# Kernel tuning notes

Hardware: AMD Instinct MI355X
Metric: run time of the kernel (lower is better)

Reference implementation:

```python
import jax, jax.numpy as jnp
import numpy as np

N = 50000        # nodes
E = 800000       # edges
R = 8            # relations
G = 64           # g_dim
H1 = 64          # h1_dim
H2 = 32          # h2_dim (per-head for transformer, output for sage)
HEADS = 4
EPS = 1e-5       # BatchNorm eps


def setup_inputs() -> dict:
    key = jax.random.key(0)
    ks = jax.random.split(key, 16)
    def rn(k, shape, scale=0.05):
        return jax.random.normal(k, shape, dtype=jnp.float32) * scale
    return {
        "node_features": jax.random.normal(ks[0], (N, G), dtype=jnp.float32),
        "node_type": jax.random.randint(ks[1], (N,), 0, 3),
        "edge_index": jax.random.randint(ks[2], (2, E), 0, N),
        "edge_type": jax.random.randint(ks[3], (E,), 0, R),
        # RGCNConv params (per-relation weight + root weight + bias)
        "rgcn_w": rn(ks[4], (R, G, H1)),
        "rgcn_root": rn(ks[5], (G, H1)),
        "rgcn_bias": jnp.zeros((H1,), jnp.float32),
        "bn1_g": jnp.ones((H1,), jnp.float32),
        "bn1_b": jnp.zeros((H1,), jnp.float32),
        # TransformerConv params (q/k/v projections + skip)
        "wq": rn(ks[6], (H1, HEADS * H2)), "bq": jnp.zeros((HEADS * H2,), jnp.float32),
        "wk": rn(ks[7], (H1, HEADS * H2)), "bk": jnp.zeros((HEADS * H2,), jnp.float32),
        "wv": rn(ks[8], (H1, HEADS * H2)), "bv": jnp.zeros((HEADS * H2,), jnp.float32),
        "wskip": rn(ks[9], (H1, HEADS * H2)), "bskip": jnp.zeros((HEADS * H2,), jnp.float32),
        "bn2_g": jnp.ones((HEADS * H2,), jnp.float32),
        "bn2_b": jnp.zeros((HEADS * H2,), jnp.float32),
        # SAGEConv params (lin_l on aggregated neighbors has bias; lin_r on root has none)
        "sage_wl": rn(ks[10], (HEADS * H2, H2)), "sage_bl": jnp.zeros((H2,), jnp.float32),
        "sage_wr": rn(ks[11], (HEADS * H2, H2)),
        "bn3_g": jnp.ones((H2,), jnp.float32),
        "bn3_b": jnp.zeros((H2,), jnp.float32),
    }


def _bn(x, g, b):
    # BatchNorm1d in training mode: biased batch statistics over nodes
    m = x.mean(0)
    v = x.var(0)
    return g * (x - m) * jax.lax.rsqrt(v + EPS) + b


def _match(res, d):
    # F.pad(res, (0, d - c)): pads with zeros if d > c, truncates if d < c
    c = res.shape[1]
    if d > c:
        return jnp.pad(res, ((0, 0), (0, d - c)))
    return res[:, :d]


def _forward(node_features, rgcn_w, rgcn_root, rgcn_bias, bn1_g, bn1_b,
             wq, bq, wk, bk, wv, bv, wskip, bskip, bn2_g, bn2_b,
             sage_wl, sage_bl, sage_wr, bn3_g, bn3_b,
             edge_index, edge_type):
    src, dst = edge_index[0], edge_index[1]
    x = node_features
    residual = x

    # ---- RGCNConv: per-relation transform, per-relation mean aggregation, sum over relations ----
    xr = jnp.einsum('nf,rfh->nrh', x, rgcn_w)            # [N,R,H1]
    msg = xr[src, edge_type]                              # [E,H1]
    seg = dst * R + edge_type                             # segment per (node, relation)
    sums = jax.ops.segment_sum(msg, seg, num_segments=N * R)
    cnt = jax.ops.segment_sum(jnp.ones((E,), msg.dtype), seg, num_segments=N * R)
    agg = (sums / jnp.maximum(cnt, 1.0)[:, None]).reshape(N, R, H1).sum(1)
    h = agg + x @ rgcn_root + rgcn_bias
    h = jax.nn.leaky_relu(_bn(h, bn1_g, bn1_b))
    x = h + _match(residual, h.shape[1])
    residual = x

    # ---- TransformerConv: edge softmax attention, concat heads, + skip projection ----
    q = (x @ wq + bq).reshape(N, HEADS, H2)
    k = (x @ wk + bk).reshape(N, HEADS, H2)
    v = (x @ wv + bv).reshape(N, HEADS, H2)
    logits = (q[dst] * k[src]).sum(-1) / jnp.sqrt(jnp.float32(H2))  # [E,HEADS]
    mx = jax.ops.segment_max(logits, dst, num_segments=N)
    ex = jnp.exp(logits - mx[dst])
    den = jax.ops.segment_sum(ex, dst, num_segments=N)
    alpha = ex / jnp.maximum(den[dst], 1e-16)
    out = jax.ops.segment_sum(alpha[:, :, None] * v[src], dst, num_segments=N)
    h = out.reshape(N, HEADS * H2) + x @ wskip + bskip
    h = jax.nn.leaky_relu(_bn(h, bn2_g, bn2_b))
    x = h + _match(residual, h.shape[1])
    residual = x

    # ---- SAGEConv: mean neighbor aggregation + root transform ----
    nsum = jax.ops.segment_sum(x[src], dst, num_segments=N)
    ncnt = jax.ops.segment_sum(jnp.ones((E,), x.dtype), dst, num_segments=N)
    nmean = nsum / jnp.maximum(ncnt, 1.0)[:, None]
    h = nmean @ sage_wl + sage_bl + x @ sage_wr
    h = jax.nn.leaky_relu(_bn(h, bn3_g, bn3_b))
    return h + _match(residual, h.shape[1])


def reference(node_features, node_type, edge_index, edge_type,
              rgcn_w, rgcn_root, rgcn_bias, bn1_g, bn1_b,
              wq, bq, wk, bk, wv, bv, wskip, bskip, bn2_g, bn2_b,
              sage_wl, sage_bl, sage_wr, bn3_g, bn3_b):
    # node_type is unused by the original forward
    return _forward(node_features, rgcn_w, rgcn_root, rgcn_bias, bn1_g, bn1_b,
                    wq, bq, wk, bk, wv, bv, wskip, bskip, bn2_g, bn2_b,
                    sage_wl, sage_bl, sage_wr, bn3_g, bn3_b,
                    edge_index, edge_type)
```

## Files before the change

kernel.cpp:

```cpp
#include <hip/hip_runtime.h>
#include <stdint.h>

#define NN 50000
#define NE 800000
#define NE4 (NE/4)
#define NR (NN*8)
#define SCAN_BS 512
#define NB2 782
#define INV_N (1.0f/50000.0f)
#define BN_EPS 1e-5f

typedef unsigned short ushort_t;
typedef unsigned char uchar_t;
typedef short bf16x8 __attribute__((ext_vector_type(8)));
typedef float f32x4 __attribute__((ext_vector_type(4)));
typedef float f32x2 __attribute__((ext_vector_type(2)));

__device__ __forceinline__ ushort_t f2bf(float f){
    unsigned int u = __float_as_uint(f);
    u += 0x7FFFu + ((u >> 16) & 1u);
    return (ushort_t)(u >> 16);
}
__device__ __forceinline__ float bf2f(ushort_t h){ return __uint_as_float(((unsigned int)h) << 16); }
__device__ __forceinline__ float bflo(unsigned int u){ return __uint_as_float(u << 16); }
__device__ __forceinline__ float bfhi(unsigned int u){ return __uint_as_float(u & 0xFFFF0000u); }

__device__ __forceinline__ unsigned int f4_to_fp8(float a, float b, float c, float d){
    int v = __builtin_amdgcn_cvt_pk_fp8_f32(a, b, 0, false);
    v = __builtin_amdgcn_cvt_pk_fp8_f32(c, d, v, true);
    return (unsigned int)v;
}
__device__ __forceinline__ void fp8_to_f4(unsigned int u, float& a, float& b, float& c, float& d){
    f32x2 lo = __builtin_amdgcn_cvt_pk_f32_fp8(u, false);
    f32x2 hi = __builtin_amdgcn_cvt_pk_f32_fp8(u, true);
    a = lo.x; b = lo.y; c = hi.x; d = hi.y;
}

__global__ void k_prep(const float* __restrict__ nf,
                       const float* __restrict__ rgcn_w, const float* __restrict__ root,
                       const float* __restrict__ wq, const float* __restrict__ wk,
                       const float* __restrict__ wv, const float* __restrict__ wsk,
                       const float* __restrict__ bq, const float* __restrict__ bk,
                       const float* __restrict__ bv, const float* __restrict__ bsk,
                       const float* __restrict__ wl, const float* __restrict__ wr,
                       const int* __restrict__ ei, const int* __restrict__ et,
                       int* __restrict__ deg, uint2* __restrict__ sr,
                       ushort_t* __restrict__ xb, uchar_t* __restrict__ xb8,
                       ushort_t* __restrict__ Wcat,
                       ushort_t* __restrict__ Wt2, float* __restrict__ bcat,
                       ushort_t* __restrict__ Wsage){
    int i = blockIdx.x*256 + threadIdx.x;
    if (i < NE4){
        int4 d = ((const int4*)(ei + NE))[i];
        int4 r = ((const int4*)et)[i];
        int s0 = d.x*8 + r.x, s1 = d.y*8 + r.y;
        int s2 = d.z*8 + r.z, s3 = d.w*8 + r.w;
        int r0 = atomicAdd(&deg[s0], 1);
        int r1 = atomicAdd(&deg[s1], 1);
        int r2 = atomicAdd(&deg[s2], 1);
        int r3 = atomicAdd(&deg[s3], 1);
        uint2* o = sr + (size_t)i*4;
        uint2 o0; o0.x = (unsigned)s0; o0.y = (unsigned)r0; o[0] = o0;
        uint2 o1; o1.x = (unsigned)s1; o1.y = (unsigned)r1; o[1] = o1;
        uint2 o2; o2.x = (unsigned)s2; o2.y = (unsigned)r2; o[2] = o2;
        uint2 o3; o3.x = (unsigned)s3; o3.y = (unsigned)r3; o[3] = o3;
        return;
    }
    int ii = i - NE4;
    const int NXB = NN*16;
    if (ii < NXB){
        float4 v = ((const float4*)nf)[ii];
        ushort4 h;
        h.x = f2bf(v.x); h.y = f2bf(v.y); h.z = f2bf(v.z); h.w = f2bf(v.w);
        ((ushort4*)xb)[ii] = h;
        ((unsigned int*)xb8)[ii] = f4_to_fp8(v.x, v.y, v.z, v.w);
        return;
    }
    int j = ii - NXB;
    if (j < 64*576){
        int h = j / 576, k = j - h*576;
        float v = (k < 512) ? rgcn_w[(size_t)k*64 + h] : root[(size_t)(k-512)*64 + h];
        Wcat[j] = f2bf(v);
    } else if (j < 64*576 + 512*64){
        int jj = j - 64*576;
        int c = jj >> 6, k = jj & 63;
        int mt = c >> 7, cc = c & 127;
        const float* W = (mt==0)?wq:(mt==1)?wk:(mt==2)?wv:wsk;
        Wt2[jj] = f2bf(W[(size_t)k*128 + cc]);
    } else if (j < 64*576 + 512*64 + 512){
        int c = j - (64*576 + 512*64);
        int mt = c >> 7, cc = c & 127;
        const float* B = (mt==0)?bq:(mt==1)?bk:(mt==2)?bv:bsk;
        bcat[c] = B[cc];
    } else if (j < 64*576 + 512*64 + 512 + 32*256){
        int jj = j - (64*576 + 512*64 + 512);
        int c = jj >> 8, k = jj & 255;
        float v = (k < 128) ? wr[(size_t)k*32 + c] : wl[(size_t)(k-128)*32 + c];
        Wsage[jj] = f2bf(v);
    }
}

__global__ void k_scan1(const int* __restrict__ deg, int* __restrict__ tmp, int* __restrict__ bsum){
    __shared__ int s[SCAN_BS];
    int t = threadIdx.x;
    int i = blockIdx.x*SCAN_BS + t;
    s[t] = (i < NR) ? deg[i] : 0;
    __syncthreads();
    for (int off = 1; off < SCAN_BS; off <<= 1){
        int add = (t >= off) ? s[t-off] : 0;
        __syncthreads();
        s[t] += add;
        __syncthreads();
    }
    if (i < NR) tmp[i] = s[t];
    if (t == SCAN_BS-1) bsum[blockIdx.x] = s[t];
}

__global__ void k_scan2(int* __restrict__ bsum){
    __shared__ int s[1024];
    int t = threadIdx.x;
    s[t] = (t < NB2) ? bsum[t] : 0;
    __syncthreads();
    for (int off = 1; off < 1024; off <<= 1){
        int v = (t >= off) ? s[t-off] : 0;
        __syncthreads();
        s[t] += v;
        __syncthreads();
    }
    if (t < NB2) bsum[t] = s[t];
}

__global__ void k_scan3(const int* __restrict__ tmp, const int* __restrict__ bsum, int* __restrict__ rs){
    int i = blockIdx.x*256 + threadIdx.x;
    if (i < NR){
        int b = i >> 9;
        int off = (b > 0) ? bsum[b-1] : 0;
        rs[i+1] = tmp[i] + off;
        if (i == 0) rs[0] = 0;
    }
}

__global__ void k_fill(const int* __restrict__ ei, const uint2* __restrict__ sr,
                       const int* __restrict__ rs, int* __restrict__ csr){
    int e = blockIdx.x*256 + threadIdx.x;
    if (e < NE){
        uint2 s = sr[e];
        csr[rs[s.x] + (int)s.y] = ei[e];
    }
}

__global__ __launch_bounds__(256) void rgcn_fused(const ushort_t* __restrict__ xb,
                                                  const uchar_t* __restrict__ xb8,
                                                  const int* __restrict__ rs,
                                                  const int* __restrict__ csr,
                                                  const ushort_t* __restrict__ Wcat,
                                                  const float* __restrict__ bias,
                                                  float* __restrict__ h1pre,
                                                  float* __restrict__ part1){
    __shared__ ushort_t Ml[16*520];
    int w = threadIdx.x >> 6, lane = threadIdx.x & 63;
    int quad = lane >> 4, l4 = lane & 15;
    int row0 = blockIdx.x * 16;
    int n0 = row0 + w*4;
    int rsel = (lane < 9 ? lane : 8);
    int rb = rs[n0*8 + rsel];
    int eb0 = __shfl(rb, 0);
    int dg0 = __shfl(rb, 8) - eb0;
    int idx = (lane < dg0) ? csr[eb0 + lane] : 0;
    for (int j = 0; j < 4; ++j){
        int lrow = (w*4 + j)*520;
        int ebase = __shfl(rb, 0);
        int enext = __shfl(rb, 8);
        int rb_next = 0, idxn = 0;
        if (j < 3){
            rb_next = rs[(n0 + j + 1)*8 + rsel];
            idxn = csr[min(enext + lane, NE - 1)];
        }
        int e0a = __shfl(rb, 2*quad);
        int e1a = __shfl(rb, 2*quad + 1);
        int e2a = __shfl(rb, 2*quad + 2);
        int oa = e0a - ebase;
        int la = e1a - e0a, lb = e2a - e1a;
        int tot = la + lb;
        int fastN = min(tot, max(64 - oa, 0));
        int ml = fastN;
        ml = max(ml, __shfl_xor(ml, 16));
        ml = max(ml, __shfl_xor(ml, 32));
        f32x2 aA0 = {0.f,0.f}, aA1 = {0.f,0.f};
        f32x2 aB0 = {0.f,0.f}, aB1 = {0.f,0.f};
        for (int i = 0; i < ml; i += 4){
            unsigned int uX[4];
#pragma unroll
            for (int u = 0; u < 4; ++u){
                int jj = i + u;
                int t = __shfl(idx, (oa + jj) & 63);
                t = (jj < fastN) ? t : 0;
                uX[u] = *(const unsigned int*)(xb8 + (size_t)t*64 + l4*4);
            }
#pragma unroll
            for (int u = 0; u < 4; ++u){
                int jj = i + u;
                unsigned int a = (jj < fastN) ? uX[u] : 0u;
                f32x2 lo = __builtin_amdgcn_cvt_pk_f32_fp8(a, false);
                f32x2 hi = __builtin_amdgcn_cvt_pk_f32_fp8(a, true);
                if (jj < la){ aA0 += lo; aA1 += hi; }
                else        { aB0 += lo; aB1 += hi; }
            }
        }
        for (int jj = min(la, fastN); jj < la; ++jj){
            int t = csr[e0a + jj];
            unsigned int a = *(const unsigned int*)(xb8 + (size_t)t*64 + l4*4);
            aA0 += __builtin_amdgcn_cvt_pk_f32_fp8(a, false);
            aA1 += __builtin_amdgcn_cvt_pk_f32_fp8(a, true);
        }
        for (int jj = max(la, fastN); jj < tot; ++jj){
            int t = csr[e0a + jj];
            unsigned int b = *(const unsigned int*)(xb8 + (size_t)t*64 + l4*4);
            aB0 += __builtin_amdgcn_cvt_pk_f32_fp8(b, false);
            aB1 += __builtin_amdgcn_cvt_pk_f32_fp8(b, true);
        }
        float inva = 1.f / fmaxf((float)la, 1.f);
        float invb = 1.f / fmaxf((float)lb, 1.f);
        ushort4 oA, oB;
        oA.x = f2bf(aA0.x*inva); oA.y = f2bf(aA0.y*inva); oA.z = f2bf(aA1.x*inva); oA.w = f2bf(aA1.y*inva);
        oB.x = f2bf(aB0.x*invb); oB.y = f2bf(aB0.y*invb); oB.z = f2bf(aB1.x*invb); oB.w = f2bf(aB1.y*invb);
        *(ushort4*)&Ml[lrow + (2*quad)*64 + l4*4] = oA;
        *(ushort4*)&Ml[lrow + (2*quad + 1)*64 + l4*4] = oB;
        if (j < 3){
            rb = rb_next;
            int ebn = __shfl(rb, 0);
            int dgn = __shfl(rb, 8) - ebn;
            idx = (lane < dgn) ? idxn : 0;
        }
    }
    __syncthreads();
    int m = l4;
    f32x4 acc = {};
#pragma unroll
    for (int kt = 0; kt < 18; ++kt){
        int kk = kt*32 + quad*8;
        bf16x8 a;
        if (kt < 16) a = *(const bf16x8*)&Ml[m*520 + kk];
        else         a = *(const bf16x8*)(xb + (size_t)(row0 + m)*64 + (kk - 512));
        bf16x8 b = *(const bf16x8*)(Wcat + (size_t)(w*16 + m)*576 + kk);
        acc = __builtin_amdgcn_mfma_f32_16x16x32_bf16(a, b, acc, 0, 0, 0);
    }
    int col = w*16 + m;
    float bz = bias[col];
    float s = 0.f, q = 0.f;
#pragma unroll
    for (int i = 0; i < 4; ++i){
        int rr = row0 + quad*4 + i;
        float y = acc[i] + bz;
        h1pre[(size_t)rr*64 + col] = y;
        s += y; q += y*y;
    }
    s += __shfl_xor(s, 16); q += __shfl_xor(q, 16);
    s += __shfl_xor(s, 32); q += __shfl_xor(q, 32);
    if (quad == 0){
        float* pg = part1 + (blockIdx.x & 31)*128;
        atomicAdd(&pg[col], s);
        atomicAdd(&pg[64 + col], q);
    }
}

#define QS 132
#define BS 68
__global__ __launch_bounds__(256) void gemm_qkvs(const float* __restrict__ h1pre,
                                                 const float* __restrict__ nf,
                                                 const float* __restrict__ part1,
                                                 const float* __restrict__ g1, const float* __restrict__ b1,
                                                 const ushort_t* __restrict__ Wt2,
                                                 const float* __restrict__ bcat,
                                                 ushort_t* __restrict__ qb,
                                                 uchar_t* __restrict__ kb8,
                                                 uchar_t* __restrict__ vb8,
                                                 ushort_t* __restrict__ sb){
    __shared__ ushort_t Bs[256*BS];
    __shared__ ushort_t pl[4][16*QS];
    __shared__ float sred[128];
    int w = threadIdx.x >> 6, lane = threadIdx.x & 63;
    int m = lane & 15, quad = lane >> 4;
    int r0 = blockIdx.x*64 + w*16;
    int row = r0 + m;
    {
        int t = threadIdx.x;
        if (t < 128){
            float acc = 0.f;
#pragma unroll
            for (int g = 0; g < 32; ++g) acc += part1[g*128 + t];
            sred[t] = acc;
        }
    }
    __syncthreads();
    bf16x8 afrag[2];
#pragma unroll
    for (int kt = 0; kt < 2; ++kt){
        int db = kt*32 + quad*8;
        bf16x8 f = (bf16x8){0,0,0,0,0,0,0,0};
        if (row < NN){
            float4 h0 = *(const float4*)(h1pre + (size_t)row*64 + db);
            float4 h1 = *(const float4*)(h1pre + (size_t)row*64 + db + 4);
            float4 n0 = *(const float4*)(nf + (size_t)row*64 + db);
            float4 n1 = *(const float4*)(nf + (size_t)row*64 + db + 4);
            float4 ga = *(const float4*)(g1 + db);
            float4 gb_ = *(const float4*)(g1 + db + 4);
            float4 ba = *(const float4*)(b1 + db);
            float4 bb_ = *(const float4*)(b1 + db + 4);
            float hh[8] = {h0.x,h0.y,h0.z,h0.w,h1.x,h1.y,h1.z,h1.w};
            float nn[8] = {n0.x,n0.y,n0.z,n0.w,n1.x,n1.y,n1.z,n1.w};
            float GG[8] = {ga.x,ga.y,ga.z,ga.w,gb_.x,gb_.y,gb_.z,gb_.w};
            float BB[8] = {ba.x,ba.y,ba.z,ba.w,bb_.x,bb_.y,bb_.z,bb_.w};
#pragma unroll
            for (int e = 0; e < 8; ++e){
                float mm = sred[db + e] * INV_N;
                float vv = sred[64 + db + e] * INV_N - mm*mm;
                float A = rsqrtf(fmaxf(vv, 0.f) + BN_EPS) * GG[e];
                float C = BB[e] - mm * A;
                float y = fmaf(hh[e], A, C);
                y = (y >= 0.f) ? y : 0.01f*y;
                f[e] = (short)f2bf(y + nn[e]);
            }
        }
        afrag[kt] = f;
    }
    for (int cg = 0; cg < 2; ++cg){
        __syncthreads();
        {
            int t = threadIdx.x;
            const ushort_t* wsrc = Wt2 + (size_t)cg*256*64;
#pragma unroll
            for (int u0 = 0; u0 < 8; ++u0){
                int u = u0*256 + t;
                int r = u >> 3, c8 = (u & 7)*8;
                *(uint4*)&Bs[r*BS + c8] = *(const uint4*)(wsrc + u*8);
            }
        }
        __syncthreads();
        f32x4 acc[16] = {};
#pragma unroll
        for (int kt = 0; kt < 2; ++kt){
            int kk = kt*32 + quad*8;
#pragma unroll
            for (int ct = 0; ct < 16; ++ct){
                bf16x8 b = *(const bf16x8*)&Bs[(size_t)(ct*16 + m)*BS + kk];
                acc[ct] = __builtin_amdgcn_mfma_f32_16x16x32_bf16(afrag[kt], b, acc[ct], 0, 0, 0);
            }
        }
#pragma unroll
        for (int ct = 0; ct < 8; ++ct){
            int g = cg*256 + ct*16 + m;
            float bz = bcat[g];
            int cc = g & 127;
#pragma unroll
            for (int i = 0; i < 4; ++i)
                pl[w][(quad*4 + i)*QS + cc] = f2bf(acc[ct][i] + bz);
        }
        if (cg == 0){
#pragma unroll
            for (int t = 0; t < 4; ++t){
                int u = t*64 + lane;
                int r = u >> 4, c = (u & 15)*8;
                int gr = r0 + r;
                if (gr < NN) *(uint4*)(qb + (size_t)gr*128 + c) = *(const uint4*)&pl[w][r*QS + c];
            }
        } else {
#pragma unroll
            for (int t = 0; t < 4; ++t){
                int u = t*64 + lane;
                int r = u >> 4, c = (u & 15)*8;
                int gr = r0 + r;
                if (gr < NN){
                    uint4 vv4 = *(const uint4*)&pl[w][r*QS + c];
                    uint2 o;
                    o.x = f4_to_fp8(bflo(vv4.x), bfhi(vv4.x), bflo(vv4.y), bfhi(vv4.y));
                    o.y = f4_to_fp8(bflo(vv4.z), bfhi(vv4.z), bflo(vv4.w), bfhi(vv4.w));
                    *(uint2*)(vb8 + (size_t)gr*128 + c) = o;
                }
            }
        }
#pragma unroll
        for (int ct = 8; ct < 16; ++ct){
            int g = cg*256 + ct*16 + m;
            float bz = bcat[g];
            int cc = g & 127;
#pragma unroll
            for (int i = 0; i < 4; ++i)
                pl[w][(quad*4 + i)*QS + cc] = f2bf(acc[ct][i] + bz);
        }
        if (cg == 0){
#pragma unroll
            for (int t = 0; t < 4; ++t){
                int u = t*64 + lane;
                int r = u >> 4, c = (u & 15)*8;
                int gr = r0 + r;
                if (gr < NN){
                    uint4 kk4 = *(const uint4*)&pl[w][r*QS + c];
                    uint2 o;
                    o.x = f4_to_fp8(bflo(kk4.x), bfhi(kk4.x), bflo(kk4.y), bfhi(kk4.y));
                    o.y = f4_to_fp8(bflo(kk4.z), bfhi(kk4.z), bflo(kk4.w), bfhi(kk4.w));
                    *(uint2*)(kb8 + (size_t)gr*128 + c) = o;
                }
            }
        } else {
#pragma unroll
            for (int t = 0; t < 4; ++t){
                int u = t*64 + lane;
                int r = u >> 4, c = (u & 15)*8;
                int gr = r0 + r;
                if (gr < NN) *(uint4*)(sb + (size_t)gr*128 + c) = *(const uint4*)&pl[w][r*QS + c];
            }
        }
    }
}

__global__ void k_red2(const float* __restrict__ part1, const float* __restrict__ part2,
                       float* __restrict__ bns){
    int t = threadIdx.x;
    float acc = 0.f;
    for (int g = 0; g < 64; ++g) acc += part2[g*256 + t];
    bns[128 + t] = acc;
    if (t < 128){
        float a1 = 0.f;
        for (int g = 0; g < 32; ++g) a1 += part1[g*128 + t];
        bns[t] = a1;
    }
}

__global__ __launch_bounds__(256) void sage_gemm(const ushort_t* __restrict__ x2b,
                                                 const ushort_t* __restrict__ nmeanb,
                                                 const ushort_t* __restrict__ Wsage,
                                                 const float* __restrict__ bl,
                                                 float* __restrict__ h3,
                                                 float* __restrict__ part3){
    int wv = threadIdx.x >> 6, lane = threadIdx.x & 63;
    int r0 = blockIdx.x*64 + wv*16;
    int m = lane & 15, quad = lane >> 4;
    int row = r0 + m;
    f32x4 acc[2] = {};
#pragma unroll
    for (int kt = 0; kt < 8; ++kt){
        int kk = kt*32 + quad*8;
        bf16x8 a;
        if (row < NN){
            const ushort_t* ap = (kt < 4) ? (x2b + (size_t)row*128 + kk)
                                          : (nmeanb + (size_t)row*128 + (kk - 128));
            a = *(const bf16x8*)ap;
        } else {
            a = (bf16x8){0,0,0,0,0,0,0,0};
        }
#pragma unroll
        for (int ct = 0; ct < 2; ++ct){
            bf16x8 b = *(const bf16x8*)(Wsage + (size_t)(ct*16 + m)*256 + kk);
            acc[ct] = __builtin_amdgcn_mfma_f32_16x16x32_bf16(a, b, acc[ct], 0, 0, 0);
        }
    }
    float s[2] = {0.f, 0.f}, q[2] = {0.f, 0.f};
#pragma unroll
    for (int ct = 0; ct < 2; ++ct){
        int col = ct*16 + m;
        float bz = bl[col];
#pragma unroll
        for (int i = 0; i < 4; ++i){
            int rr = r0 + quad*4 + i;
            if (rr < NN){
                float y = acc[ct][i] + bz;
                h3[(size_t)rr*32 + col] = y;
                s[ct] += y; q[ct] += y*y;
            }
        }
    }
#pragma unroll
    for (int ct = 0; ct < 2; ++ct){
        s[ct] += __shfl_xor(s[ct], 16); q[ct] += __shfl_xor(q[ct], 16);
        s[ct] += __shfl_xor(s[ct], 32); q[ct] += __shfl_xor(q[ct], 32);
    }
    if (quad == 0){
        float* pg = part3 + (blockIdx.x & 3)*64;
#pragma unroll
        for (int ct = 0; ct < 2; ++ct){
            int col = ct*16 + m;
            atomicAdd(&pg[col], s[ct]);
            atomicAdd(&pg[32 + col], q[ct]);
        }
    }
}

__device__ __forceinline__ float bn_leaky(float z, float m, float rsv, float g, float b){
    float y = (z - m) * rsv * g + b;
    return y >= 0.f ? y : 0.01f * y;
}

__global__ void bn_apply2(const float* __restrict__ h2, const float* __restrict__ h1pre,
                          const float* __restrict__ nf,
                          const float* __restrict__ g1, const float* __restrict__ b1,
                          const float* __restrict__ s1, const float* __restrict__ q1,
                          const float* __restrict__ g2, const float* __restrict__ b2,
                          const float* __restrict__ s2, const float* __restrict__ q2,
                          float* __restrict__ x2r, ushort_t* __restrict__ x2b,
                          uchar_t* __restrict__ x28){
    int i = blockIdx.x*256 + threadIdx.x;
    if (i >= NN*128) return;
    int n = i >> 7, c = i & 127;
    float m2 = s2[c] * INV_N;
    float v2 = q2[c] * INV_N - m2*m2;
    float rsv2 = rsqrtf(fmaxf(v2, 0.f) + BN_EPS);
    float val = bn_leaky(h2[i], m2, rsv2, g2[c], b2[c]);
    if (c < 64){
        float m1 = s1[c] * INV_N;
        float v1 = q1[c] * INV_N - m1*m1;
        float rsv1 = rsqrtf(fmaxf(v1, 0.f) + BN_EPS);
        val += bn_leaky(h1pre[(size_t)n*64 + c], m1, rsv1, g1[c], b1[c]) + nf[(size_t)n*64 + c];
    }
    if (c < 32) x2r[(size_t)n*32 + c] = val;
    x2b[i] = f2bf(val);
    int p = __builtin_amdgcn_cvt_pk_fp8_f32(val, val, 0, false);
    x28[i] = (uchar_t)(p & 0xFF);
}

__global__ void bn_apply3(const float* __restrict__ h3, const float* __restrict__ x2r,
                          const float* __restrict__ g, const float* __restrict__ b,
                          const float* __restrict__ part3,
                          float* __restrict__ out){
    int i = blockIdx.x*256 + threadIdx.x;
    if (i >= NN*32) return;
    int c = i & 31;
    float s = 0.f, q = 0.f;
#pragma unroll
    for (int gg = 0; gg < 4; ++gg){
        s += part3[gg*64 + c];
        q += part3[gg*64 + 32 + c];
    }
    float m = s * INV_N;
    float v = q * INV_N - m*m;
    float rsv = rsqrtf(fmaxf(v, 0.f) + BN_EPS);
    out[i] = bn_leaky(h3[i], m, rsv, g[c], b[c]) + x2r[i];
}

__global__ __launch_bounds__(256) void attn_kernel(const ushort_t* __restrict__ qb,
                                                   const uchar_t* __restrict__ kb8,
                                                   const uchar_t* __restrict__ vb8,
                                                   const ushort_t* __restrict__ sb,
                                                   const int* __restrict__ rs,
                                                   const int* __restrict__ csr,
                                                   float* __restrict__ h2,
                                                   float* __restrict__ part2){
    __shared__ float sm[2][4][128];
    int w = threadIdx.x >> 6, lane = threadIdx.x & 63;
    int n = blockIdx.x*4 + w;
    int half = lane >> 5, l5 = lane & 31;
    int e0 = rs[n*8], e1 = rs[n*8 + 8];
    int deg = e1 - e0;
    uint2 qu = *(const uint2*)(qb + (size_t)n*128 + l5*4);
    uint2 sbv = *(const uint2*)(sb + (size_t)n*128 + l5*4);
    float q0 = bflo(qu.x), q1 = bfhi(qu.x), q2 = bflo(qu.y), q3 = bfhi(qu.y);
    const float scale = 0.17677669529663687f;
    int idx = 0;
    if (lane < deg) idx = csr[e0 + lane];
    int dcap = min(deg, 64);
    int nt = (dcap + 7) >> 3;
    float den = 0.f, a0 = 0.f, a1 = 0.f, a2 = 0.f, a3 = 0.f;
    for (int t = 0; t < nt; ++t){
        int i2 = t*8 + half*4;
        int j0 = i2, j1 = i2+1, j2 = i2+2, j3 = i2+3;
        bool v0 = j0 < dcap, v1 = j1 < dcap, v2 = j2 < dcap, v3 = j3 < dcap;
        int s0 = __shfl(idx, j0 & 63); s0 = v0 ? s0 : 0;
        int s1 = __shfl(idx, j1 & 63); s1 = v1 ? s1 : 0;
        int s2 = __shfl(idx, j2 & 63); s2 = v2 ? s2 : 0;
        int s3 = __shfl(idx, j3 & 63); s3 = v3 ? s3 : 0;
        unsigned int ku0 = *(const unsigned int*)(kb8 + (size_t)s0*128 + l5*4);
        unsigned int ku1 = *(const unsigned int*)(kb8 + (size_t)s1*128 + l5*4);
        unsigned int ku2 = *(const unsigned int*)(kb8 + (size_t)s2*128 + l5*4);
        unsigned int ku3 = *(const unsigned int*)(kb8 + (size_t)s3*128 + l5*4);
        unsigned int vu0 = *(const unsigned int*)(vb8 + (size_t)s0*128 + l5*4);
        unsigned int vu1 = *(const unsigned int*)(vb8 + (size_t)s1*128 + l5*4);
        unsigned int vu2 = *(const unsigned int*)(vb8 + (size_t)s2*128 + l5*4);
        unsigned int vu3 = *(const unsigned int*)(vb8 + (size_t)s3*128 + l5*4);
        float ka, kb_, kc, kd;
        fp8_to_f4(ku0, ka, kb_, kc, kd);
        float p0 = q0*ka + q1*kb_ + q2*kc + q3*kd;
        fp8_to_f4(ku1, ka, kb_, kc, kd);
        float p1 = q0*ka + q1*kb_ + q2*kc + q3*kd;
        fp8_to_f4(ku2, ka, kb_, kc, kd);
        float p2 = q0*ka + q1*kb_ + q2*kc + q3*kd;
        fp8_to_f4(ku3, ka, kb_, kc, kd);
        float p3 = q0*ka + q1*kb_ + q2*kc + q3*kd;
        p0 += __shfl_xor(p0, 1); p1 += __shfl_xor(p1, 1); p2 += __shfl_xor(p2, 1); p3 += __shfl_xor(p3, 1);
        p0 += __shfl_xor(p0, 2); p1 += __shfl_xor(p1, 2); p2 += __shfl_xor(p2, 2); p3 += __shfl_xor(p3, 2);
        p0 += __shfl_xor(p0, 4); p1 += __shfl_xor(p1, 4); p2 += __shfl_xor(p2, 4); p3 += __shfl_xor(p3, 4);
        float w0 = v0 ? __expf(p0 * scale) : 0.f;
        float w1 = v1 ? __expf(p1 * scale) : 0.f;
        float w2 = v2 ? __expf(p2 * scale) : 0.f;
        float w3 = v3 ? __expf(p3 * scale) : 0.f;
        den += w0 + w1 + w2 + w3;
        float va, vb_, vc, vd;
        fp8_to_f4(vu0, va, vb_, vc, vd);
        a0 = fmaf(w0, va, a0); a1 = fmaf(w0, vb_, a1); a2 = fmaf(w0, vc, a2); a3 = fmaf(w0, vd, a3);
        fp8_to_f4(vu1, va, vb_, vc, vd);
        a0 = fmaf(w1, va, a0); a1 = fmaf(w1, vb_, a1); a2 = fmaf(w1, vc, a2); a3 = fmaf(w1, vd, a3);
        fp8_to_f4(vu2, va, vb_, vc, vd);
        a0 = fmaf(w2, va, a0); a1 = fmaf(w2, vb_, a1); a2 = fmaf(w2, vc, a2); a3 = fmaf(w2, vd, a3);
        fp8_to_f4(vu3, va, vb_, vc, vd);
        a0 = fmaf(w3, va, a0); a1 = fmaf(w3, vb_, a1); a2 = fmaf(w3, vc, a2); a3 = fmaf(w3, vd, a3);
    }
    for (int e = 64 + half; e < deg; e += 2){
        int s = csr[e0 + e];
        unsigned int ku = *(const unsigned int*)(kb8 + (size_t)s*128 + l5*4);
        unsigned int vu = *(const unsigned int*)(vb8 + (size_t)s*128 + l5*4);
        float ka, kb_, kc, kd;
        fp8_to_f4(ku, ka, kb_, kc, kd);
        float p = q0*ka + q1*kb_ + q2*kc + q3*kd;
        p += __shfl_xor(p, 1);
        p += __shfl_xor(p, 2);
        p += __shfl_xor(p, 4);
        float wg = __expf(p * scale);
        den += wg;
        float va, vb_, vc, vd;
        fp8_to_f4(vu, va, vb_, vc, vd);
        a0 = fmaf(wg, va, a0); a1 = fmaf(wg, vb_, a1); a2 = fmaf(wg, vc, a2); a3 = fmaf(wg, vd, a3);
    }
    den += __shfl_xor(den, 32);
    a0 += __shfl_xor(a0, 32); a1 += __shfl_xor(a1, 32);
    a2 += __shfl_xor(a2, 32); a3 += __shfl_xor(a3, 32);
    float inv = (den > 0.f) ? 1.f/den : 0.f;
    float o0 = bflo(sbv.x) + a0*inv;
    float o1 = bfhi(sbv.x) + a1*inv;
    float o2 = bflo(sbv.y) + a2*inv;
    float o3 = bfhi(sbv.y) + a3*inv;
    if (half == 0){
        float4 o; o.x = o0; o.y = o1; o.z = o2; o.w = o3;
        *(float4*)(h2 + (size_t)n*128 + l5*4) = o;
        float4 t; t.x = o0; t.y = o1; t.z = o2; t.w = o3;
        *(float4*)&sm[0][w][l5*4] = t;
    } else {
        float4 t; t.x = o0*o0; t.y = o1*o1; t.z = o2*o2; t.w = o3*o3;
        *(float4*)&sm[1][w][l5*4] = t;
    }
    __syncthreads();
    {
        int t = threadIdx.x;
        int st = t >> 7, c = t & 127;
        float v = sm[st][0][c] + sm[st][1][c] + sm[st][2][c] + sm[st][3][c];
        atomicAdd(&part2[(blockIdx.x & 63)*256 + st*128 + c], v);
    }
}

__global__ __launch_bounds__(256) void sage_agg(const uchar_t* __restrict__ x28,
                                                const int* __restrict__ rs,
                                                const int* __restrict__ csr,
                                                ushort_t* __restrict__ nmeanb){
    int w = threadIdx.x >> 6, lane = threadIdx.x & 63;
    int n = blockIdx.x*4 + w;
    if (n >= NN) return;
    int half = lane >> 5, l5 = lane & 31;
    int e0 = rs[n*8], e1 = rs[n*8 + 8];
    int deg = e1 - e0;
    int idx = 0;
    if (lane < deg) idx = csr[e0 + lane];
    int dcap = min(deg, 64);
    int nt = (dcap + 7) >> 3;
    f32x2 A0 = {0.f,0.f}, A1 = {0.f,0.f};
    for (int t = 0; t < nt; ++t){
        int i2 = t*8 + half*4;
        int j0 = i2, j1 = i2+1, j2 = i2+2, j3 = i2+3;
        bool v0 = j0 < dcap, v1 = j1 < dcap, v2 = j2 < dcap, v3 = j3 < dcap;
        int s0 = __shfl(idx, j0 & 63); s0 = v0 ? s0 : 0;
        int s1 = __shfl(idx, j1 & 63); s1 = v1 ? s1 : 0;
        int s2 = __shfl(idx, j2 & 63); s2 = v2 ? s2 : 0;
        int s3 = __shfl(idx, j3 & 63); s3 = v3 ? s3 : 0;
        unsigned int u0 = *(const unsigned int*)(x28 + (size_t)s0*128 + l5*4);
        unsigned int u1 = *(const unsigned int*)(x28 + (size_t)s1*128 + l5*4);
        unsigned int u2 = *(const unsigned int*)(x28 + (size_t)s2*128 + l5*4);
        unsigned int u3 = *(const unsigned int*)(x28 + (size_t)s3*128 + l5*4);
        u0 = v0 ? u0 : 0u; u1 = v1 ? u1 : 0u;
        u2 = v2 ? u2 : 0u; u3 = v3 ? u3 : 0u;
        A0 += __builtin_amdgcn_cvt_pk_f32_fp8(u0, false);
        A1 += __builtin_amdgcn_cvt_pk_f32_fp8(u0, true);
        A0 += __builtin_amdgcn_cvt_pk_f32_fp8(u1, false);
        A1 += __builtin_amdgcn_cvt_pk_f32_fp8(u1, true);
        A0 += __builtin_amdgcn_cvt_pk_f32_fp8(u2, false);
        A1 += __builtin_amdgcn_cvt_pk_f32_fp8(u2, true);
        A0 += __builtin_amdgcn_cvt_pk_f32_fp8(u3, false);
        A1 += __builtin_amdgcn_cvt_pk_f32_fp8(u3, true);
    }
    for (int e = 64 + half; e < deg; e += 2){
        int s = csr[e0 + e];
        unsigned int u = *(const unsigned int*)(x28 + (size_t)s*128 + l5*4);
        A0 += __builtin_amdgcn_cvt_pk_f32_fp8(u, false);
        A1 += __builtin_amdgcn_cvt_pk_f32_fp8(u, true);
    }
    float a0 = A0.x, a1 = A0.y, a2 = A1.x, a3 = A1.y;
    a0 += __shfl_xor(a0, 32); a1 += __shfl_xor(a1, 32);
    a2 += __shfl_xor(a2, 32); a3 += __shfl_xor(a3, 32);
    if (half == 0){
        float inv = 1.f / fmaxf((float)deg, 1.f);
        ushort4 o;
        o.x = f2bf(a0*inv); o.y = f2bf(a1*inv); o.z = f2bf(a2*inv); o.w = f2bf(a3*inv);
        *(ushort4*)(nmeanb + (size_t)n*128 + l5*4) = o;
    }
}

extern "C" void kernel_launch(void* const* d_in, const int* in_sizes, int n_in,
                              void* d_out, int out_size, void* d_ws, size_t ws_size,
                              hipStream_t stream){
    const float* nf      = (const float*)d_in[0];
    const int*   ei      = (const int*)d_in[2];
    const int*   et      = (const int*)d_in[3];
    const float* rgcn_w  = (const float*)d_in[4];
    const float* root    = (const float*)d_in[5];
    const float* rbias   = (const float*)d_in[6];
    const float* bn1g    = (const float*)d_in[7];
    const float* bn1b    = (const float*)d_in[8];
    const float* wq      = (const float*)d_in[9];
    const float* bq      = (const float*)d_in[10];
    const float* wk      = (const float*)d_in[11];
    const float* bk      = (const float*)d_in[12];
    const float* wv      = (const float*)d_in[13];
    const float* bv      = (const float*)d_in[14];
    const float* wsk     = (const float*)d_in[15];
    const float* bsk     = (const float*)d_in[16];
    const float* bn2g    = (const float*)d_in[17];
    const float* bn2b    = (const float*)d_in[18];
    const float* wl      = (const float*)d_in[19];
    const float* bl      = (const float*)d_in[20];
    const float* wr      = (const float*)d_in[21];
    const float* bn3g    = (const float*)d_in[22];
    const float* bn3b    = (const float*)d_in[23];
    float* out = (float*)d_out;

    char* base = (char*)d_ws;
    size_t off = 0;
    auto take = [&](size_t bytes) -> char* {
        char* p = base + off;
        off += (bytes + 255) & ~(size_t)255;
        return p;
    };
    int*      deg    = (int*)take((size_t)NR*4);
    float*    bns    = (float*)take(1024*4);
    float*    part1  = (float*)take(32*128*4);
    float*    part2  = (float*)take(64*256*4);
    float*    part3  = (float*)take(4*64*4);
    char*     zend   = base + off;
    int*      rs     = (int*)take((size_t)(NR+1)*4);
    int*      tmp    = (int*)take((size_t)NR*4);
    int*      bsum   = (int*)take(1024*4);
    uint2*    sr     = (uint2*)take((size_t)NE*8);
    int*      csr    = (int*)take((size_t)NE*4);
    ushort_t* Wcat   = (ushort_t*)take(64*576*2);
    ushort_t* Wt2    = (ushort_t*)take(512*64*2);
    float*    bcat   = (float*)take(512*4);
    ushort_t* Wsage  = (ushort_t*)take(32*256*2);
    ushort_t* xb     = (ushort_t*)take((size_t)NN*64*2);
    uchar_t*  xb8    = (uchar_t*)take((size_t)NN*64);
    float*    h1pre  = (float*)take((size_t)NN*64*4);
    float*    h2     = (float*)take((size_t)NN*128*4);
    float*    x2r    = (float*)take((size_t)NN*32*4);
    ushort_t* sb     = (ushort_t*)take((size_t)NN*128*2);
    char*     bigA   = take((size_t)NN*512*2);
    if (off > ws_size) return;

    ushort_t* qb     = (ushort_t*)(bigA + (size_t)NN*128);
    uchar_t*  vb8    = (uchar_t*)(bigA + (size_t)NN*384);
    uchar_t*  kb8    = (uchar_t*)(bigA + (size_t)NN*640);
    ushort_t* x2b    = (ushort_t*)bigA;
    uchar_t*  x28    = (uchar_t*)(bigA + (size_t)NN*256);
    ushort_t* nmeanb = (ushort_t*)(bigA + (size_t)NN*512);
    float*    h3     = (float*)(bigA + (size_t)NN*768);

    hipMemsetAsync(deg, 0, (size_t)(zend - (char*)deg), stream);

    const int PREP_N = NE4 + NN*16 + 64*576 + 512*64 + 512 + 32*256;
    k_prep <<<(PREP_N+255)/256, 256, 0, stream>>>(nf, rgcn_w, root, wq, wk, wv, wsk,
                                                  bq, bk, bv, bsk, wl, wr,
                                                  ei, et, deg, sr,
                                                  xb, xb8, Wcat, Wt2, bcat, Wsage);
    k_scan1<<<NB2, SCAN_BS, 0, stream>>>(deg, tmp, bsum);
    k_scan2<<<1, 1024, 0, stream>>>(bsum);
    k_scan3<<<(NR+255)/256, 256, 0, stream>>>(tmp, bsum, rs);
    k_fill <<<(NE+255)/256, 256, 0, stream>>>(ei, sr, rs, csr);

    const int NB4 = (NN + 3) / 4;
    const int NBG = (NN + 63) / 64;

    rgcn_fused<<<NN/16, 256, 0, stream>>>(xb, xb8, rs, csr, Wcat, rbias, h1pre, part1);

    gemm_qkvs<<<NBG, 256, 0, stream>>>(h1pre, nf, part1, bn1g, bn1b,
                                       Wt2, bcat, qb, kb8, vb8, sb);
    attn_kernel<<<NB4, 256, 0, stream>>>(qb, kb8, vb8, sb, rs, csr, h2, part2);
    k_red2<<<1, 256, 0, stream>>>(part1, part2, bns);
    bn_apply2<<<(NN*128+255)/256, 256, 0, stream>>>(h2, h1pre, nf,
                                                    bn1g, bn1b, bns + 0, bns + 64,
                                                    bn2g, bn2b, bns + 128, bns + 256,
                                                    x2r, x2b, x28);

    sage_agg<<<NB4, 256, 0, stream>>>(x28, rs, csr, nmeanb);
    sage_gemm<<<NBG, 256, 0, stream>>>(x2b, nmeanb, Wsage, bl, h3, part3);
    bn_apply3<<<(NN*32+255)/256, 256, 0, stream>>>(h3, x2r, bn3g, bn3b, part3, out);
}
```

Before: 363.4 us.

## Process eight edges per prep thread, fold scan2 into scan3, halve rgcn rows per block

The prep kernel now handles eight edges per thread instead of four, which cuts the thread count for degree counting. The single-block scan2 kernel is removed. scan3 now computes each block's offset by reducing the preceding bsum entries itself, so it does redundant work per block but saves one launch. The fused RGCN kernel processes 8 rows per block instead of 16, which doubles the block count for better occupancy and latency hiding. In exchange, half of each 16-row MFMA tile is duplicated and wasted.

```diff
diff --git a/kernel.cpp b/kernel.cpp
--- a/kernel.cpp
+++ b/kernel.cpp
@@ -3,7 +3,7 @@
 
 #define NN 50000
 #define NE 800000
-#define NE4 (NE/4)
+#define NE8 (NE/8)
 #define NR (NN*8)
 #define SCAN_BS 512
 #define NB2 782
@@ -50,23 +50,28 @@
                        ushort_t* __restrict__ Wt2, float* __restrict__ bcat,
                        ushort_t* __restrict__ Wsage){
     int i = blockIdx.x*256 + threadIdx.x;
-    if (i < NE4){
-        int4 d = ((const int4*)(ei + NE))[i];
-        int4 r = ((const int4*)et)[i];
-        int s0 = d.x*8 + r.x, s1 = d.y*8 + r.y;
-        int s2 = d.z*8 + r.z, s3 = d.w*8 + r.w;
-        int r0 = atomicAdd(&deg[s0], 1);
-        int r1 = atomicAdd(&deg[s1], 1);
-        int r2 = atomicAdd(&deg[s2], 1);
-        int r3 = atomicAdd(&deg[s3], 1);
-        uint2* o = sr + (size_t)i*4;
-        uint2 o0; o0.x = (unsigned)s0; o0.y = (unsigned)r0; o[0] = o0;
-        uint2 o1; o1.x = (unsigned)s1; o1.y = (unsigned)r1; o[1] = o1;
-        uint2 o2; o2.x = (unsigned)s2; o2.y = (unsigned)r2; o[2] = o2;
-        uint2 o3; o3.x = (unsigned)s3; o3.y = (unsigned)r3; o[3] = o3;
+    if (i < NE8){
+        const int4* dp = (const int4*)(ei + NE);
+        const int4* rp = (const int4*)et;
+        int4 d0 = dp[i*2], d1 = dp[i*2 + 1];
+        int4 r0 = rp[i*2], r1 = rp[i*2 + 1];
+        int sg[8];
+        sg[0] = d0.x*8 + r0.x; sg[1] = d0.y*8 + r0.y;
+        sg[2] = d0.z*8 + r0.z; sg[3] = d0.w*8 + r0.w;
+        sg[4] = d1.x*8 + r1.x; sg[5] = d1.y*8 + r1.y;
+        sg[6] = d1.z*8 + r1.z; sg[7] = d1.w*8 + r1.w;
+        int rk[8];
+#pragma unroll
+        for (int u = 0; u < 8; ++u) rk[u] = atomicAdd(&deg[sg[u]], 1);
+        uint2* o = sr + (size_t)i*8;
+#pragma unroll
+        for (int u = 0; u < 8; ++u){
+            uint2 ov; ov.x = (unsigned)sg[u]; ov.y = (unsigned)rk[u];
+            o[u] = ov;
+        }
         return;
     }
-    int ii = i - NE4;
+    int ii = i - NE8;
     const int NXB = NN*16;
     if (ii < NXB){
         float4 v = ((const float4*)nf)[ii];
@@ -116,25 +121,22 @@
     if (t == SCAN_BS-1) bsum[blockIdx.x] = s[t];
 }
 
-__global__ void k_scan2(int* __restrict__ bsum){
-    __shared__ int s[1024];
+__global__ void k_scan3(const int* __restrict__ tmp, const int* __restrict__ bsum, int* __restrict__ rs){
+    __shared__ int sacc[256];
+    int B = blockIdx.x;
+    int b = B >> 1;
     int t = threadIdx.x;
-    s[t] = (t < NB2) ? bsum[t] : 0;
+    int acc = 0;
+    for (int g = t; g < b; g += 256) acc += bsum[g];
+    sacc[t] = acc;
     __syncthreads();
-    for (int off = 1; off < 1024; off <<= 1){
-        int v = (t >= off) ? s[t-off] : 0;
+    for (int off2 = 128; off2 > 0; off2 >>= 1){
+        if (t < off2) sacc[t] += sacc[t + off2];
         __syncthreads();
-        s[t] += v;
-        __syncthreads();
-    }
-    if (t < NB2) bsum[t] = s[t];
-}
-
-__global__ void k_scan3(const int* __restrict__ tmp, const int* __restrict__ bsum, int* __restrict__ rs){
-    int i = blockIdx.x*256 + threadIdx.x;
+    }
+    int off = sacc[0];
+    int i = B*256 + t;
     if (i < NR){
-        int b = i >> 9;
-        int off = (b > 0) ? bsum[b-1] : 0;
         rs[i+1] = tmp[i] + off;
         if (i == 0) rs[0] = 0;
     }
@@ -157,22 +159,22 @@
                                                   const float* __restrict__ bias,
                                                   float* __restrict__ h1pre,
                                                   float* __restrict__ part1){
-    __shared__ ushort_t Ml[16*520];
+    __shared__ ushort_t Ml[8*520];
     int w = threadIdx.x >> 6, lane = threadIdx.x & 63;
     int quad = lane >> 4, l4 = lane & 15;
-    int row0 = blockIdx.x * 16;
-    int n0 = row0 + w*4;
+    int row0 = blockIdx.x * 8;
+    int n0 = row0 + w*2;
     int rsel = (lane < 9 ? lane : 8);
     int rb = rs[n0*8 + rsel];
     int eb0 = __shfl(rb, 0);
     int dg0 = __shfl(rb, 8) - eb0;
     int idx = (lane < dg0) ? csr[eb0 + lane] : 0;
-    for (int j = 0; j < 4; ++j){
-        int lrow = (w*4 + j)*520;
+    for (int j = 0; j < 2; ++j){
+        int lrow = (w*2 + j)*520;
         int ebase = __shfl(rb, 0);
         int enext = __shfl(rb, 8);
         int rb_next = 0, idxn = 0;
-        if (j < 3){
+        if (j < 1){
             rb_next = rs[(n0 + j + 1)*8 + rsel];
             idxn = csr[min(enext + lane, NE - 1)];
         }
@@ -226,7 +228,7 @@
         oB.x = f2bf(aB0.x*invb); oB.y = f2bf(aB0.y*invb); oB.z = f2bf(aB1.x*invb); oB.w = f2bf(aB1.y*invb);
         *(ushort4*)&Ml[lrow + (2*quad)*64 + l4*4] = oA;
         *(ushort4*)&Ml[lrow + (2*quad + 1)*64 + l4*4] = oB;
-        if (j < 3){
+        if (j < 1){
             rb = rb_next;
             int ebn = __shfl(rb, 0);
             int dgn = __shfl(rb, 8) - ebn;
@@ -235,13 +237,14 @@
     }
     __syncthreads();
     int m = l4;
+    int m8 = m & 7;
     f32x4 acc = {};
 #pragma unroll
     for (int kt = 0; kt < 18; ++kt){
         int kk = kt*32 + quad*8;
         bf16x8 a;
-        if (kt < 16) a = *(const bf16x8*)&Ml[m*520 + kk];
-        else         a = *(const bf16x8*)(xb + (size_t)(row0 + m)*64 + (kk - 512));
+        if (kt < 16) a = *(const bf16x8*)&Ml[m8*520 + kk];
+        else         a = *(const bf16x8*)(xb + (size_t)(row0 + m8)*64 + (kk - 512));
         bf16x8 b = *(const bf16x8*)(Wcat + (size_t)(w*16 + m)*576 + kk);
         acc = __builtin_amdgcn_mfma_f32_16x16x32_bf16(a, b, acc, 0, 0, 0);
     }
@@ -250,10 +253,12 @@
     float s = 0.f, q = 0.f;
 #pragma unroll
     for (int i = 0; i < 4; ++i){
-        int rr = row0 + quad*4 + i;
-        float y = acc[i] + bz;
-        h1pre[(size_t)rr*64 + col] = y;
-        s += y; q += y*y;
+        int r = quad*4 + i;
+        if (r < 8){
+            float y = acc[i] + bz;
+            h1pre[(size_t)(row0 + r)*64 + col] = y;
+            s += y; q += y*y;
+        }
     }
     s += __shfl_xor(s, 16); q += __shfl_xor(q, 16);
     s += __shfl_xor(s, 32); q += __shfl_xor(q, 32);
@@ -769,20 +774,19 @@
 
     hipMemsetAsync(deg, 0, (size_t)(zend - (char*)deg), stream);
 
-    const int PREP_N = NE4 + NN*16 + 64*576 + 512*64 + 512 + 32*256;
+    const int PREP_N = NE8 + NN*16 + 64*576 + 512*64 + 512 + 32*256;
     k_prep <<<(PREP_N+255)/256, 256, 0, stream>>>(nf, rgcn_w, root, wq, wk, wv, wsk,
                                                   bq, bk, bv, bsk, wl, wr,
                                                   ei, et, deg, sr,
                                                   xb, xb8, Wcat, Wt2, bcat, Wsage);
     k_scan1<<<NB2, SCAN_BS, 0, stream>>>(deg, tmp, bsum);
-    k_scan2<<<1, 1024, 0, stream>>>(bsum);
     k_scan3<<<(NR+255)/256, 256, 0, stream>>>(tmp, bsum, rs);
     k_fill <<<(NE+255)/256, 256, 0, stream>>>(ei, sr, rs, csr);
 
     const int NB4 = (NN + 3) / 4;
     const int NBG = (NN + 63) / 64;
 
-    rgcn_fused<<<NN/16, 256, 0, stream>>>(xb, xb8, rs, csr, Wcat, rbias, h1pre, part1);
+    rgcn_fused<<<NN/8, 256, 0, stream>>>(xb, xb8, rs, csr, Wcat, rbias, h1pre, part1);
 
     gemm_qkvs<<<NBG, 256, 0, stream>>>(h1pre, nf, part1, bn1g, bn1b,
                                        Wt2, bcat, qb, kb8, vb8, sb);
```

Result: slower. 386.7 us (+6.4%).
